# Optimization experiments

Measured on AMD Instinct MI355X. Metric: run time of the kernel, lower is better.

## Reference

```python
import jax, jax.numpy as jnp
import numpy as np

N = 50000      # nodes
E = 800000     # edges (before self-loops)
IN = 128       # in_channels
HID = 32       # hidden_channels
H = 4          # num_heads
OUT = 2        # out_channels
NEG_SLOPE = 0.2


def setup_inputs() -> dict:
    key = jax.random.key(0)
    ks = jax.random.split(key, 16)
    s = 0.1
    x = jax.random.normal(ks[0], (N, IN), jnp.float32)
    edge_index = jax.random.randint(ks[1], (2, E), 0, N, dtype=jnp.int32)
    W1 = jax.random.normal(ks[2], (IN, H * HID), jnp.float32) * s
    att_src1 = jax.random.normal(ks[3], (H, HID), jnp.float32) * s
    att_dst1 = jax.random.normal(ks[4], (H, HID), jnp.float32) * s
    b1 = jnp.zeros((H * HID,), jnp.float32)
    W2 = jax.random.normal(ks[5], (H * HID, H * HID), jnp.float32) * s
    att_src2 = jax.random.normal(ks[6], (H, HID), jnp.float32) * s
    att_dst2 = jax.random.normal(ks[7], (H, HID), jnp.float32) * s
    b2 = jnp.zeros((H * HID,), jnp.float32)
    W3 = jax.random.normal(ks[8], (H * HID, OUT), jnp.float32) * s
    att_src3 = jax.random.normal(ks[9], (1, OUT), jnp.float32) * s
    att_dst3 = jax.random.normal(ks[10], (1, OUT), jnp.float32) * s
    b3 = jnp.zeros((OUT,), jnp.float32)
    return {"x": x, "edge_index": edge_index,
            "W1": W1, "att_src1": att_src1, "att_dst1": att_dst1, "b1": b1,
            "W2": W2, "att_src2": att_src2, "att_dst2": att_dst2, "b2": b2,
            "W3": W3, "att_src3": att_src3, "att_dst3": att_dst3, "b3": b3}


def gat_layer(x, src, dst, W, a_src, a_dst, b, heads, ch, concat):
    """PyG GATConv (eval mode): per-edge LeakyReLU attention, edge-softmax over
    incoming edges of each destination node, weighted scatter-add aggregation."""
    n = x.shape[0]
    h = (x @ W).reshape(n, heads, ch)                      # [N,H,C]
    alpha_s = jnp.sum(h * a_src, axis=-1)                  # [N,H]
    alpha_d = jnp.sum(h * a_dst, axis=-1)                  # [N,H]
    alpha = jax.nn.leaky_relu(alpha_s[src] + alpha_d[dst], NEG_SLOPE)  # [E',H]
    amax = jax.ops.segment_max(alpha, dst, num_segments=n)             # [N,H]
    e = jnp.exp(alpha - amax[dst])
    denom = jax.ops.segment_sum(e, dst, num_segments=n)
    w = e / denom[dst]                                     # softmax weights [E',H]
    out = jax.ops.segment_sum(h[src] * w[:, :, None], dst, num_segments=n)  # [N,H,C]
    out = out.reshape(n, heads * ch) if concat else out.mean(axis=1)
    return out + b


def reference(x, edge_index, W1, att_src1, att_dst1, b1,
              W2, att_src2, att_dst2, b2, W3, att_src3, att_dst3, b3):
    # PyG GATConv adds self-loops by default
    loop = jnp.arange(N, dtype=edge_index.dtype)
    src = jnp.concatenate([edge_index[0], loop])
    dst = jnp.concatenate([edge_index[1], loop])
    h = jax.nn.elu(gat_layer(x, src, dst, W1, att_src1, att_dst1, b1, H, HID, True))
    h = jax.nn.elu(gat_layer(h, src, dst, W2, att_src2, att_dst2, b2, H, HID, True))
    h = gat_layer(h, src, dst, W3, att_src3, att_dst3, b3, 1, OUT, False)
    return jax.nn.log_softmax(h, axis=1)
```

## Files before the change

### kernel.cpp

```cpp
#include <hip/hip_runtime.h>
#include <hip/hip_fp16.h>

#define NN 50000
#define EE 800000
#define ET 850000
#define NEG 0.2f
#define SCAN_B 1024
#define NBLK ((NN + SCAN_B - 1) / SCAN_B)

__device__ __forceinline__ float leaky(float x) { return fmaxf(x, NEG * x); }
__device__ __forceinline__ float elu_f(float x) { return x > 0.f ? x : expm1f(x); }

struct alignas(8) half4 { __half2 a, b; };

typedef _Float16 half8_t __attribute__((ext_vector_type(8)));
typedef float float4_t __attribute__((ext_vector_type(4)));

__global__ void hist_k(const int* __restrict__ ei, int* __restrict__ counts,
                       int* __restrict__ rank) {
    int i = blockIdx.x * blockDim.x + threadIdx.x;
    if (i >= ET) return;
    int dst = (i < EE) ? ei[EE + i] : (i - EE);
    rank[i] = atomicAdd(&counts[dst], 1);
}

__global__ void scan1_k(const int* __restrict__ counts, int* __restrict__ rp,
                        int* __restrict__ bsums) {
    __shared__ int lsum[256];
    int base = blockIdx.x * SCAN_B;
    int v[4];
    int tsum = 0;
#pragma unroll
    for (int j = 0; j < 4; ++j) {
        int i = base + threadIdx.x * 4 + j;
        v[j] = (i < NN) ? counts[i] : 0;
        tsum += v[j];
    }
    lsum[threadIdx.x] = tsum;
    __syncthreads();
    for (int off = 1; off < 256; off <<= 1) {
        int t = (threadIdx.x >= off) ? lsum[threadIdx.x - off] : 0;
        __syncthreads();
        lsum[threadIdx.x] += t;
        __syncthreads();
    }
    int excl = lsum[threadIdx.x] - tsum;
#pragma unroll
    for (int j = 0; j < 4; ++j) {
        int i = base + threadIdx.x * 4 + j;
        if (i < NN) rp[i] = excl;
        excl += v[j];
    }
    if (threadIdx.x == 255) bsums[blockIdx.x] = lsum[255];
}

__global__ void scan2_k(int* __restrict__ bsums, int* __restrict__ rp) {
    int lane = threadIdx.x;
    int v = (lane < NBLK) ? bsums[lane] : 0;
    int orig = v;
    for (int off = 1; off < 64; off <<= 1) {
        int t = __shfl_up(v, off, 64);
        if (lane >= off) v += t;
    }
    if (lane < NBLK) bsums[lane] = v - orig;
    if (lane == 63) rp[NN] = v;
}

__global__ void scan3_k(int* __restrict__ rp, const int* __restrict__ bsums) {
    int add = bsums[blockIdx.x];
    int base = blockIdx.x * SCAN_B + threadIdx.x * 4;
#pragma unroll
    for (int j = 0; j < 4; ++j) {
        int i = base + j;
        if (i < NN) rp[i] += add;
    }
}

__global__ void scatter_k(const int* __restrict__ ei, const int* __restrict__ rp,
                          const int* __restrict__ rank, int* __restrict__ csr) {
    int i = blockIdx.x * blockDim.x + threadIdx.x;
    if (i >= ET) return;
    int src, dst;
    if (i < EE) { src = ei[i]; dst = ei[EE + i]; }
    else        { src = dst = i - EE; }
    csr[rp[dst] + rank[i]] = src;
}

__global__ void wt_k(const float* __restrict__ W, __half* __restrict__ Wt) {
    int i = blockIdx.x * 256 + threadIdx.x;
    int k = i >> 7, n = i & 127;
    Wt[n * 128 + k] = __float2half(W[i]);
}

__global__ __launch_bounds__(256)
void gemm_mfma_k(const float* __restrict__ Xf, const __half* __restrict__ Xh,
                 const __half* __restrict__ Wt, __half* __restrict__ Yh, int nrows,
                 const float* __restrict__ att_s, const float* __restrict__ att_d,
                 float* __restrict__ asb, float* __restrict__ adb) {
    int lane = threadIdx.x & 63;
    int wid  = threadIdx.x >> 6;
    int n = lane & 15, quad = lane >> 4;
    float atts_r[8], attd_r[8];
#pragma unroll
    for (int t = 0; t < 8; ++t) {
        atts_r[t] = att_s[t * 16 + n];
        attd_r[t] = att_d[t * 16 + n];
    }
    for (int row0 = (blockIdx.x * 4 + wid) * 16; row0 < nrows; row0 += gridDim.x * 64) {
        float4_t acc[8];
#pragma unroll
        for (int t = 0; t < 8; ++t) acc[t] = (float4_t){0.f, 0.f, 0.f, 0.f};
        int rA = row0 + n; if (rA >= nrows) rA = nrows - 1;
#pragma unroll
        for (int ch = 0; ch < 4; ++ch) {
            half8_t a;
            if (Xh) {
                a = *(const half8_t*)(Xh + (size_t)rA * 128 + ch * 32 + quad * 8);
            } else {
                const float* xp = Xf + (size_t)rA * 128 + ch * 32 + quad * 8;
                float4 f0 = *(const float4*)xp;
                float4 f1 = *(const float4*)(xp + 4);
                a = (half8_t){(_Float16)f0.x, (_Float16)f0.y, (_Float16)f0.z, (_Float16)f0.w,
                              (_Float16)f1.x, (_Float16)f1.y, (_Float16)f1.z, (_Float16)f1.w};
            }
#pragma unroll
            for (int t = 0; t < 8; ++t) {
                half8_t b = *(const half8_t*)(Wt + (t * 16 + n) * 128 + ch * 32 + quad * 8);
                acc[t] = __builtin_amdgcn_mfma_f32_16x16x32_f16(a, b, acc[t], 0, 0, 0);
            }
        }
#pragma unroll
        for (int rg = 0; rg < 4; ++rg) {
            int row = row0 + quad * 4 + rg;
            if (row < nrows) {
                __half* yp = Yh + (size_t)row * 128 + n;
#pragma unroll
                for (int t = 0; t < 8; ++t)
                    yp[t * 16] = __float2half(acc[t][rg]);
            }
        }
#pragma unroll
        for (int rg = 0; rg < 4; ++rg) {
            float ps[4], pd[4];
#pragma unroll
            for (int h = 0; h < 4; ++h) {
                ps[h] = acc[2*h][rg] * atts_r[2*h] + acc[2*h+1][rg] * atts_r[2*h+1];
                pd[h] = acc[2*h][rg] * attd_r[2*h] + acc[2*h+1][rg] * attd_r[2*h+1];
#pragma unroll
                for (int mask = 1; mask < 16; mask <<= 1) {
                    ps[h] += __shfl_xor(ps[h], mask, 64);
                    pd[h] += __shfl_xor(pd[h], mask, 64);
                }
            }
            int row = row0 + quad * 4 + rg;
            if (n == 0 && row < nrows) {
#pragma unroll
                for (int h = 0; h < 4; ++h) {
                    asb[row * 4 + h] = ps[h];
                    adb[row * 4 + h] = pd[h];
                }
            }
        }
    }
}

__global__ __launch_bounds__(256)
void agg_k(const __half* __restrict__ Hh, const float* __restrict__ asb,
           const float* __restrict__ adb, const int* __restrict__ rp,
           const int* __restrict__ csr, const float* __restrict__ bias,
           __half* __restrict__ Y,
           const float* __restrict__ W3, const float* __restrict__ s3w,
           const float* __restrict__ d3w, float* __restrict__ h3,
           float* __restrict__ as3, float* __restrict__ ad3) {
    int lane = threadIdx.x & 63;
    int hw = lane >> 5;
    int l  = lane & 31;
    int n = blockIdx.x * 8 + (threadIdx.x >> 6) * 2 + hw;
    if (n >= NN) return;
    int hd = l >> 3;
    float ad = adb[n * 4 + hd];
    float acc0 = 0.f, acc1 = 0.f, acc2 = 0.f, acc3 = 0.f, den = 0.f;
    int e = rp[n], end = rp[n + 1], last = end - 1;
    for (int base = e; base < end; base += 8) {
        int s[8]; float a[8]; float2 hraw[8];
#pragma unroll
        for (int j = 0; j < 8; ++j) {
            int i = base + j;
            s[j] = csr[i <= last ? i : last];
        }
#pragma unroll
        for (int j = 0; j < 8; ++j) a[j] = asb[s[j] * 4 + hd] + ad;
#pragma unroll
        for (int j = 0; j < 8; ++j)
            hraw[j] = ((const float2*)(Hh + (size_t)s[j] * 128))[l];
#pragma unroll
        for (int j = 0; j < 8; ++j) {
            float w = __expf(leaky(a[j]));
            w = (base + j <= last) ? w : 0.f;
            den += w;
            const __half2* hp = (const __half2*)&hraw[j];
            float2 f01 = __half22float2(hp[0]);
            float2 f23 = __half22float2(hp[1]);
            acc0 += w * f01.x; acc1 += w * f01.y;
            acc2 += w * f23.x; acc3 += w * f23.y;
        }
    }
    float4 bv = ((const float4*)bias)[l];
    float inv = 1.f / den;
    float o0 = elu_f(acc0 * inv + bv.x);
    float o1 = elu_f(acc1 * inv + bv.y);
    float o2 = elu_f(acc2 * inv + bv.z);
    float o3 = elu_f(acc3 * inv + bv.w);
    if (!W3) {
        half4 hv;
        hv.a = __floats2half2_rn(o0, o1);
        hv.b = __floats2half2_rn(o2, o3);
        ((half4*)(Y + (size_t)n * 128))[l] = hv;
    } else {
        float4 wa = ((const float4*)W3)[l * 2];
        float4 wb = ((const float4*)W3)[l * 2 + 1];
        float p0 = o0 * wa.x + o1 * wa.z + o2 * wb.x + o3 * wb.z;
        float p1 = o0 * wa.y + o1 * wa.w + o2 * wb.y + o3 * wb.w;
        for (int off = 16; off > 0; off >>= 1) {
            p0 += __shfl_down(p0, off, 32);
            p1 += __shfl_down(p1, off, 32);
        }
        if (l == 0) {
            h3[n * 2 + 0] = p0;
            h3[n * 2 + 1] = p1;
            as3[n] = p0 * s3w[0] + p1 * s3w[1];
            ad3[n] = p0 * d3w[0] + p1 * d3w[1];
        }
    }
}

__global__ void l3agg_k(const float* __restrict__ h3, const float* __restrict__ as3,
                        const float* __restrict__ ad3, const int* __restrict__ rp,
                        const int* __restrict__ csr, const float* __restrict__ b3,
                        float* __restrict__ out) {
    int n = blockIdx.x * blockDim.x + threadIdx.x;
    if (n >= NN) return;
    const float2* h2 = (const float2*)h3;
    float adn = ad3[n];
    float den = 0.f, a0 = 0.f, a1 = 0.f;
    int e = rp[n], end = rp[n + 1], last = end - 1;
    for (int base = e; base < end; base += 4) {
        int s[4]; float al[4]; float2 g[4];
#pragma unroll
        for (int j = 0; j < 4; ++j) {
            int i = base + j;
            s[j] = csr[i <= last ? i : last];
        }
#pragma unroll
        for (int j = 0; j < 4; ++j) al[j] = as3[s[j]] + adn;
#pragma unroll
        for (int j = 0; j < 4; ++j) g[j] = h2[s[j]];
#pragma unroll
        for (int j = 0; j < 4; ++j) {
            float w = __expf(leaky(al[j]));
            w = (base + j <= last) ? w : 0.f;
            den += w;
            a0 += w * g[j].x;
            a1 += w * g[j].y;
        }
    }
    float o0 = a0 / den + b3[0];
    float o1 = a1 / den + b3[1];
    float m = fmaxf(o0, o1);
    float lse = m + logf(__expf(o0 - m) + __expf(o1 - m));
    out[n * 2 + 0] = o0 - lse;
    out[n * 2 + 1] = o1 - lse;
}

extern "C" void kernel_launch(void* const* d_in, const int* in_sizes, int n_in,
                              void* d_out, int out_size, void* d_ws, size_t ws_size,
                              hipStream_t stream) {
    const float* x   = (const float*)d_in[0];
    const int*   ei  = (const int*)d_in[1];
    const float* W1  = (const float*)d_in[2];
    const float* as1 = (const float*)d_in[3];
    const float* ad1 = (const float*)d_in[4];
    const float* b1  = (const float*)d_in[5];
    const float* W2  = (const float*)d_in[6];
    const float* as2 = (const float*)d_in[7];
    const float* ad2 = (const float*)d_in[8];
    const float* b2  = (const float*)d_in[9];
    const float* W3  = (const float*)d_in[10];
    const float* s3w = (const float*)d_in[11];
    const float* d3w = (const float*)d_in[12];
    const float* b3  = (const float*)d_in[13];
    float* out = (float*)d_out;

    char* ws = (char*)d_ws;
    size_t off = 0;
    auto alloc = [&](size_t bytes) -> char* {
        char* p = ws + off;
        off = (off + bytes + 255) & ~(size_t)255;
        return p;
    };
    __half* hA    = (__half*)alloc((size_t)NN * 128 * 2);
    __half* hBh   = (__half*)alloc((size_t)NN * 128 * 2);
    float* asb    = (float*)alloc((size_t)NN * 4 * 4);
    float* adb    = (float*)alloc((size_t)NN * 4 * 4);
    int*   rp     = (int*)alloc((size_t)(NN + 1) * 4);
    int*   counts = (int*)alloc((size_t)NN * 4);
    int*   csr    = (int*)alloc((size_t)ET * 4);
    int*   rank   = (int*)alloc((size_t)ET * 4);
    int*   bsums  = (int*)alloc((size_t)NBLK * 4);
    __half* Wt1   = (__half*)alloc(128 * 128 * 2);
    __half* Wt2   = (__half*)alloc(128 * 128 * 2);
    float* h3     = (float*)alloc((size_t)NN * 2 * 4);
    float* s3     = (float*)alloc((size_t)NN * 4);
    float* d3     = (float*)alloc((size_t)NN * 4);

    wt_k<<<64, 256, 0, stream>>>(W1, Wt1);
    wt_k<<<64, 256, 0, stream>>>(W2, Wt2);

    hipMemsetAsync(counts, 0, (size_t)NN * 4, stream);
    hist_k<<<(ET + 255) / 256, 256, 0, stream>>>(ei, counts, rank);
    scan1_k<<<NBLK, 256, 0, stream>>>(counts, rp, bsums);
    scan2_k<<<1, 64, 0, stream>>>(bsums, rp);
    scan3_k<<<NBLK, 256, 0, stream>>>(rp, bsums);
    scatter_k<<<(ET + 255) / 256, 256, 0, stream>>>(ei, rp, rank, csr);

    gemm_mfma_k<<<(NN + 63) / 64, 256, 0, stream>>>(x, nullptr, Wt1, hA, NN,
                                                    as1, ad1, asb, adb);
    agg_k<<<(NN + 7) / 8, 256, 0, stream>>>(hA, asb, adb, rp, csr, b1, hBh,
                                            nullptr, nullptr, nullptr,
                                            nullptr, nullptr, nullptr);

    gemm_mfma_k<<<(NN + 63) / 64, 256, 0, stream>>>(nullptr, hBh, Wt2, hA, NN,
                                                    as2, ad2, asb, adb);
    agg_k<<<(NN + 7) / 8, 256, 0, stream>>>(hA, asb, adb, rp, csr, b2, nullptr,
                                            W3, s3w, d3w, h3, s3, d3);

    l3agg_k<<<(NN + 255) / 256, 256, 0, stream>>>(h3, s3, d3, rp, csr, b3, out);
}
```

Before: 290.6 us.

## Stage GEMM output via LDS, use nontemporal loads, widen aggregation batch, merge weight transposes

Several unrelated changes. The GEMM output is staged through shared memory so each row is written with coalesced 16-byte stores, and the grid-stride loop is dropped in favour of one tile per wave. Streaming edge and input reads use nontemporal loads and stores. The aggregation kernel batches 16 neighbours per iteration instead of 8 to raise memory-level parallelism, which costs more registers and wastes lanes on low-degree nodes. The two weight-transpose launches are merged into one.

```diff
diff --git a/kernel.cpp b/kernel.cpp
--- a/kernel.cpp
+++ b/kernel.cpp
@@ -20,8 +20,9 @@
                        int* __restrict__ rank) {
     int i = blockIdx.x * blockDim.x + threadIdx.x;
     if (i >= ET) return;
-    int dst = (i < EE) ? ei[EE + i] : (i - EE);
-    rank[i] = atomicAdd(&counts[dst], 1);
+    int dst = (i < EE) ? __builtin_nontemporal_load(ei + EE + i) : (i - EE);
+    int r = atomicAdd(&counts[dst], 1);
+    __builtin_nontemporal_store(r, rank + i);
 }
 
 __global__ void scan1_k(const int* __restrict__ counts, int* __restrict__ rp,
@@ -81,15 +82,24 @@
     int i = blockIdx.x * blockDim.x + threadIdx.x;
     if (i >= ET) return;
     int src, dst;
-    if (i < EE) { src = ei[i]; dst = ei[EE + i]; }
-    else        { src = dst = i - EE; }
-    csr[rp[dst] + rank[i]] = src;
-}
-
-__global__ void wt_k(const float* __restrict__ W, __half* __restrict__ Wt) {
+    if (i < EE) {
+        src = __builtin_nontemporal_load(ei + i);
+        dst = __builtin_nontemporal_load(ei + EE + i);
+    } else {
+        src = dst = i - EE;
+    }
+    int r = __builtin_nontemporal_load(rank + i);
+    csr[rp[dst] + r] = src;
+}
+
+__global__ void wt_k(const float* __restrict__ W1, const float* __restrict__ W2,
+                     __half* __restrict__ Wt1, __half* __restrict__ Wt2) {
     int i = blockIdx.x * 256 + threadIdx.x;
-    int k = i >> 7, n = i & 127;
-    Wt[n * 128 + k] = __float2half(W[i]);
+    const float* W = (i < 16384) ? W1 : W2;
+    __half* Wt = (i < 16384) ? Wt1 : Wt2;
+    int j = i & 16383;
+    int k = j >> 7, n = j & 127;
+    Wt[n * 128 + k] = __float2half(W[j]);
 }
 
 __global__ __launch_bounds__(256)
@@ -97,68 +107,82 @@
                  const __half* __restrict__ Wt, __half* __restrict__ Yh, int nrows,
                  const float* __restrict__ att_s, const float* __restrict__ att_d,
                  float* __restrict__ asb, float* __restrict__ adb) {
+    __shared__ __align__(16) __half cst[4][16 * 128];
     int lane = threadIdx.x & 63;
     int wid  = threadIdx.x >> 6;
     int n = lane & 15, quad = lane >> 4;
+    int row0 = (blockIdx.x * 4 + wid) * 16;
+
     float atts_r[8], attd_r[8];
 #pragma unroll
     for (int t = 0; t < 8; ++t) {
         atts_r[t] = att_s[t * 16 + n];
         attd_r[t] = att_d[t * 16 + n];
     }
-    for (int row0 = (blockIdx.x * 4 + wid) * 16; row0 < nrows; row0 += gridDim.x * 64) {
-        float4_t acc[8];
-#pragma unroll
-        for (int t = 0; t < 8; ++t) acc[t] = (float4_t){0.f, 0.f, 0.f, 0.f};
-        int rA = row0 + n; if (rA >= nrows) rA = nrows - 1;
-#pragma unroll
-        for (int ch = 0; ch < 4; ++ch) {
-            half8_t a;
-            if (Xh) {
-                a = *(const half8_t*)(Xh + (size_t)rA * 128 + ch * 32 + quad * 8);
-            } else {
-                const float* xp = Xf + (size_t)rA * 128 + ch * 32 + quad * 8;
-                float4 f0 = *(const float4*)xp;
-                float4 f1 = *(const float4*)(xp + 4);
-                a = (half8_t){(_Float16)f0.x, (_Float16)f0.y, (_Float16)f0.z, (_Float16)f0.w,
-                              (_Float16)f1.x, (_Float16)f1.y, (_Float16)f1.z, (_Float16)f1.w};
+
+    float4_t acc[8];
+#pragma unroll
+    for (int t = 0; t < 8; ++t) acc[t] = (float4_t){0.f, 0.f, 0.f, 0.f};
+    int rA = row0 + n; if (rA >= nrows) rA = nrows - 1;
+#pragma unroll
+    for (int ch = 0; ch < 4; ++ch) {
+        half8_t a;
+        if (Xh) {
+            a = __builtin_nontemporal_load(
+                    (const half8_t*)(Xh + (size_t)rA * 128 + ch * 32 + quad * 8));
+        } else {
+            const float4_t* xp = (const float4_t*)(Xf + (size_t)rA * 128 + ch * 32 + quad * 8);
+            float4_t f0 = __builtin_nontemporal_load(xp);
+            float4_t f1 = __builtin_nontemporal_load(xp + 1);
+            a = (half8_t){(_Float16)f0.x, (_Float16)f0.y, (_Float16)f0.z, (_Float16)f0.w,
+                          (_Float16)f1.x, (_Float16)f1.y, (_Float16)f1.z, (_Float16)f1.w};
+        }
+#pragma unroll
+        for (int t = 0; t < 8; ++t) {
+            half8_t b = *(const half8_t*)(Wt + (t * 16 + n) * 128 + ch * 32 + quad * 8);
+            acc[t] = __builtin_amdgcn_mfma_f32_16x16x32_f16(a, b, acc[t], 0, 0, 0);
+        }
+    }
+
+#pragma unroll
+    for (int rg = 0; rg < 4; ++rg) {
+        float ps[4], pd[4];
+#pragma unroll
+        for (int h = 0; h < 4; ++h) {
+            ps[h] = acc[2*h][rg] * atts_r[2*h] + acc[2*h+1][rg] * atts_r[2*h+1];
+            pd[h] = acc[2*h][rg] * attd_r[2*h] + acc[2*h+1][rg] * attd_r[2*h+1];
+#pragma unroll
+            for (int mask = 1; mask < 16; mask <<= 1) {
+                ps[h] += __shfl_xor(ps[h], mask, 64);
+                pd[h] += __shfl_xor(pd[h], mask, 64);
             }
-#pragma unroll
-            for (int t = 0; t < 8; ++t) {
-                half8_t b = *(const half8_t*)(Wt + (t * 16 + n) * 128 + ch * 32 + quad * 8);
-                acc[t] = __builtin_amdgcn_mfma_f32_16x16x32_f16(a, b, acc[t], 0, 0, 0);
+        }
+        int row = row0 + quad * 4 + rg;
+        if (n == 0 && row < nrows) {
+#pragma unroll
+            for (int h = 0; h < 4; ++h) {
+                asb[row * 4 + h] = ps[h];
+                adb[row * 4 + h] = pd[h];
             }
         }
-#pragma unroll
-        for (int rg = 0; rg < 4; ++rg) {
-            int row = row0 + quad * 4 + rg;
-            if (row < nrows) {
-                __half* yp = Yh + (size_t)row * 128 + n;
-#pragma unroll
-                for (int t = 0; t < 8; ++t)
-                    yp[t * 16] = __float2half(acc[t][rg]);
-            }
-        }
-#pragma unroll
-        for (int rg = 0; rg < 4; ++rg) {
-            float ps[4], pd[4];
-#pragma unroll
-            for (int h = 0; h < 4; ++h) {
-                ps[h] = acc[2*h][rg] * atts_r[2*h] + acc[2*h+1][rg] * atts_r[2*h+1];
-                pd[h] = acc[2*h][rg] * attd_r[2*h] + acc[2*h+1][rg] * attd_r[2*h+1];
-#pragma unroll
-                for (int mask = 1; mask < 16; mask <<= 1) {
-                    ps[h] += __shfl_xor(ps[h], mask, 64);
-                    pd[h] += __shfl_xor(pd[h], mask, 64);
-                }
-            }
-            int row = row0 + quad * 4 + rg;
-            if (n == 0 && row < nrows) {
-#pragma unroll
-                for (int h = 0; h < 4; ++h) {
-                    asb[row * 4 + h] = ps[h];
-                    adb[row * 4 + h] = pd[h];
-                }
+    }
+
+#pragma unroll
+    for (int rg = 0; rg < 4; ++rg)
+#pragma unroll
+        for (int t = 0; t < 8; ++t)
+            cst[wid][(quad * 4 + rg) * 128 + t * 16 + n] = __float2half(acc[t][rg]);
+    __syncthreads();
+    {
+        int chunk = lane & 15;
+        int rsub  = lane >> 4;
+#pragma unroll
+        for (int it = 0; it < 4; ++it) {
+            int row = it * 4 + rsub;
+            int grow = row0 + row;
+            if (grow < nrows) {
+                half8_t v = *(const half8_t*)(&cst[wid][row * 128 + chunk * 8]);
+                *(half8_t*)(Yh + (size_t)grow * 128 + chunk * 8) = v;
             }
         }
     }
@@ -181,20 +205,20 @@
     float ad = adb[n * 4 + hd];
     float acc0 = 0.f, acc1 = 0.f, acc2 = 0.f, acc3 = 0.f, den = 0.f;
     int e = rp[n], end = rp[n + 1], last = end - 1;
-    for (int base = e; base < end; base += 8) {
-        int s[8]; float a[8]; float2 hraw[8];
-#pragma unroll
-        for (int j = 0; j < 8; ++j) {
+    for (int base = e; base < end; base += 16) {
+        int s[16]; float a[16]; float2 hraw[16];
+#pragma unroll
+        for (int j = 0; j < 16; ++j) {
             int i = base + j;
             s[j] = csr[i <= last ? i : last];
         }
 #pragma unroll
-        for (int j = 0; j < 8; ++j) a[j] = asb[s[j] * 4 + hd] + ad;
-#pragma unroll
-        for (int j = 0; j < 8; ++j)
+        for (int j = 0; j < 16; ++j) a[j] = asb[s[j] * 4 + hd] + ad;
+#pragma unroll
+        for (int j = 0; j < 16; ++j)
             hraw[j] = ((const float2*)(Hh + (size_t)s[j] * 128))[l];
 #pragma unroll
-        for (int j = 0; j < 8; ++j) {
+        for (int j = 0; j < 16; ++j) {
             float w = __expf(leaky(a[j]));
             w = (base + j <= last) ? w : 0.f;
             den += w;
@@ -313,8 +337,7 @@
     float* s3     = (float*)alloc((size_t)NN * 4);
     float* d3     = (float*)alloc((size_t)NN * 4);
 
-    wt_k<<<64, 256, 0, stream>>>(W1, Wt1);
-    wt_k<<<64, 256, 0, stream>>>(W2, Wt2);
+    wt_k<<<128, 256, 0, stream>>>(W1, W2, Wt1, Wt2);
 
     hipMemsetAsync(counts, 0, (size_t)NN * 4, stream);
     hist_k<<<(ET + 255) / 256, 256, 0, stream>>>(ei, counts, rank);
```

Result: slower. 306.0 us (+5.3%).
